# Performance work log

Hardware: AMD Instinct MI355X
Metric: run time of the kernel (lower is better)

## Reference

```python
import jax, jax.numpy as jnp
import numpy as np

LMAX = 4
S2_DIM = (LMAX + 1) ** 2                                  # 25: s2 irreps, mul 1 per l
SO3_DIM = sum((2 * l + 1) ** 2 for l in range(LMAX + 1))  # 165: so3 irreps, mul 2l+1 per l
B = 2048
F_S2, F_SO3 = 1, 16
N_S2_KERNEL = 48      # s2_healpix_grid(rec_level=1)
N_SO3_KERNEL = 192    # so3_near_identity_grid()
N_ACT_GRID = 4000     # SO3Activation resolution=10, aspect_ratio=2 -> 20x10x20, flattened
N_EVAL = 4608         # so3_healpix_grid(rec_level=2): 192 pixels x 24 gamma


def setup_inputs() -> dict:
    ks = jax.random.split(jax.random.key(0), 7)
    return {
        "x": jax.random.normal(ks[0], (B, F_S2, S2_DIM), jnp.float32),
        "w_s2": jax.random.normal(ks[1], (F_S2, F_SO3, N_S2_KERNEL), jnp.float32),
        "Y": jax.random.normal(ks[2], (N_S2_KERNEL, S2_DIM), jnp.float32),
        "w_so3": jax.random.normal(ks[3], (F_SO3, 1, N_SO3_KERNEL), jnp.float32),
        "D_kernel": jax.random.normal(ks[4], (N_SO3_KERNEL, SO3_DIM), jnp.float32),
        "D_act": jax.random.normal(ks[5], (N_ACT_GRID, SO3_DIM), jnp.float32),
        "eval_wigners": jax.random.normal(ks[6], (SO3_DIM, N_EVAL), jnp.float32) / np.sqrt(SO3_DIM),
    }


def _s2_to_so3_linear(x, psi):
    # e3nn o3.Linear(s2_irreps -> so3_irreps, f_in, f_out, external weights)
    # x:   [B, f_in, 25]  (mul 1 per degree l)
    # psi: [f_in, f_out, 25] ; column l^2+j is the weight to output-multiplicity j of degree l
    f_in, f_out = psi.shape[0], psi.shape[1]
    out, s = [], 0
    for l in range(LMAX + 1):
        d = 2 * l + 1
        x_l = x[..., s:s + d]                       # [B, f_in, d]
        p_l = psi[..., s:s + d]                     # [f_in, f_out, d] (j = out-mul idx)
        o = jnp.einsum('bxm,xyj->byjm', x_l, p_l) / np.sqrt(f_in)
        out.append(o.reshape(x.shape[0], f_out, d * d))
        s += d
    return jnp.concatenate(out, axis=-1)            # [B, f_out, 165]


def _so3_to_so3_linear(x, psi):
    # e3nn o3.Linear(so3_irreps -> so3_irreps, f_in, f_out, external weights)
    # x:   [B, f_in, 165] ; psi: [f_in, f_out, 165]
    f_in, f_out = psi.shape[0], psi.shape[1]
    out, s = [], 0
    for l in range(LMAX + 1):
        d = 2 * l + 1
        x_l = x[..., s:s + d * d].reshape(x.shape[0], f_in, d, d)   # [B,f_in,u,m]
        p_l = psi[..., s:s + d * d].reshape(f_in, f_out, d, d)      # [f_in,f_out,u,v]
        o = jnp.einsum('bxum,xyuv->byvm', x_l, p_l) / np.sqrt(f_in * d)
        out.append(o.reshape(x.shape[0], f_out, d * d))
        s += d * d
    return jnp.concatenate(out, axis=-1)            # [B, f_out, 165]


def _forward(x, w_s2, Y, w_so3, D_kernel, D_act, eval_wigners):
    # --- S2Convolution: kernel = SH-transform of grid weights, then irrep-wise linear
    psi1 = jnp.einsum('ni,xyn->xyi', Y, w_s2) / np.sqrt(N_S2_KERNEL)     # [1,16,25]
    h = _s2_to_so3_linear(x, psi1)                                        # [B,16,165]
    # --- SO3Activation: Fourier -> SO(3) grid -> relu -> Fourier
    g = jnp.einsum('bfi,gi->bfg', h, D_act) / np.sqrt(SO3_DIM)            # [B,16,4000]
    g = jax.nn.relu(g)
    h = jnp.einsum('bfg,gi->bfi', g, D_act) * (np.sqrt(SO3_DIM) / N_ACT_GRID)
    # --- SO3Convolution
    psi2 = jnp.einsum('ni,xyn->xyi', D_kernel, w_so3) / np.sqrt(N_SO3_KERNEL)  # [16,1,165]
    harmonics = _so3_to_so3_linear(h, psi2)                               # [B,1,165]
    # --- compute_probabilities: matmul with eval Wigner-D basis + softmax over grid
    probs = jax.nn.softmax(jnp.einsum('bfi,ie->be', harmonics, eval_wigners), axis=1)  # [B,4608]
    # --- top-k masking: zero out everything below the 5th-highest prob of sample 0
    fifth = jax.lax.top_k(probs, 5)[0][0, 4]
    probs = jnp.where(probs < fifth, 0.0, probs)
    return harmonics, probs


def reference(x, w_s2, Y, w_so3, D_kernel, D_act, eval_wigners):
    return _forward(x, w_s2, Y, w_so3, D_kernel, D_act, eval_wigners)
```

## Files before the change

kernel.cpp:

```cpp
#include <hip/hip_runtime.h>

typedef short bf16x8 __attribute__((ext_vector_type(8)));
typedef float f32x16 __attribute__((ext_vector_type(16)));
typedef int   i32x4  __attribute__((ext_vector_type(4)));

#define INV_SQRT165 0.07784989441615349f
#define FINAL_SCALE 0.0032113081446662823f
#define ZERO16 ((f32x16){0.f,0.f,0.f,0.f,0.f,0.f,0.f,0.f,0.f,0.f,0.f,0.f,0.f,0.f,0.f,0.f})

__device__ __forceinline__ unsigned short f2bf(float f) {
  unsigned int u = __builtin_bit_cast(unsigned int, f);
  unsigned int r = (u + 0x7FFFu + ((u >> 16) & 1u)) >> 16;
  return (unsigned short)r;
}
__device__ __forceinline__ float bf2f(unsigned short h) {
  unsigned int u = ((unsigned int)h) << 16;
  return __builtin_bit_cast(float, u);
}
__device__ __forceinline__ unsigned int pack_bf2f(float lo, float hi) {
  unsigned int a = (__builtin_bit_cast(unsigned int, lo) + 0x8000u) >> 16;
  unsigned int b = (__builtin_bit_cast(unsigned int, hi) + 0x8000u) & 0xFFFF0000u;
  return b | a;
}

__device__ __forceinline__ void gl_lds16(const void* g, void* l) {
  __builtin_amdgcn_global_load_lds(
      (const __attribute__((address_space(1))) unsigned int*)(unsigned long long)g,
      (__attribute__((address_space(3))) unsigned int*)(unsigned int)(unsigned long long)l,
      16, 0, 0);
}

__device__ __forceinline__ void decode_i(int i, int& lv, int& rel) {
  if (i < 1)       { lv = 0; rel = i; }
  else if (i < 10) { lv = 1; rel = i - 1; }
  else if (i < 35) { lv = 2; rel = i - 10; }
  else if (i < 84) { lv = 3; rel = i - 35; }
  else             { lv = 4; rel = i - 84; }
}
__device__ __forceinline__ int divq(int rel, int lv) {
  const int mag[5] = {32768, 10923, 6554, 4682, 3641};
  return (rel * mag[lv]) >> 15;
}

__device__ __forceinline__ int gperm(int p) {
  int a = p & 3, hlp = (p >> 2) & 1, c = p >> 3;
  return ((c >> 1) << 4) + hlp * 8 + ((c & 1) << 2) + a;
}

__global__ __launch_bounds__(256) void prep_k(const float* __restrict__ Da,
                                              const float* __restrict__ ew,
                                              const float* __restrict__ Y,
                                              const float* __restrict__ w_s2,
                                              const float* __restrict__ Dk,
                                              const float* __restrict__ w_so3,
                                              unsigned short* __restrict__ e1pre,
                                              unsigned short* __restrict__ d2pre,
                                              unsigned short* __restrict__ ewpre,
                                              float* __restrict__ psi2) {
  __shared__ __align__(16) unsigned short lds[13824];
  const int tid = threadIdx.x;
  const int l = tid & 63, hl = l >> 5, ln = l & 31;
  if (blockIdx.x < 128) {
    const int ci = blockIdx.x, g0 = ci * 32;
    float* psi1L = (float*)(lds + 6464);
    for (int e = tid; e < 6400; e += 256) lds[e] = 0;
    for (int e = tid; e < 400; e += 256) {
      int yv = e / 25, iv = e % 25;
      float s = 0.f;
      for (int n = 0; n < 48; n++) s += Y[n * 25 + iv] * w_s2[yv * 48 + n];
      psi1L[e] = s * 0.14433756729740643f;
    }
    __syncthreads();
    int rows = 4000 - g0; if (rows > 32) rows = 32; if (rows < 0) rows = 0;
    int ne = rows * 165;
    for (int e = tid; e < ne; e += 256) {
      int gl_ = e / 165, k = e - gl_ * 165;
      lds[gl_ * 200 + k] = f2bf(Da[g0 * 165 + e]);
    }
    __syncthreads();
#pragma unroll
    for (int it = 0; it < 3; it++) {
      int tt = it * 4 + (tid >> 6);
      int nf = tt >> 1, gk = tt & 1;
      unsigned short v[8];
#pragma unroll
      for (int j = 0; j < 8; j++)
        v[j] = lds[(gk * 16 + hl * 8 + j) * 200 + nf * 32 + ln];
      *(i32x4*)(d2pre + ci * 6144 + tt * 512 + l * 8) = *(i32x4*)v;
    }
    for (int yy = 0; yy < 16; yy++) {
#pragma unroll
      for (int it = 0; it < 4; it++) {
        int idx = it * 256 + tid;
        int kf = idx >> 9, r2 = idx & 511;
        int ll = r2 >> 3, j = r2 & 7;
        int lnn = ll & 31, hll = ll >> 5;
        int k = kf * 16 + hll * 8 + j;
        unsigned short ov = 0;
        if (k < 25) {
          int lv = (k < 1) ? 0 : (k < 4) ? 1 : (k < 9) ? 2 : (k < 16) ? 3 : 4;
          int d = 2 * lv + 1;
          int m = k - lv * lv;
          int off165 = lv * (4 * lv * lv - 1) / 3;
          int gp = gperm(lnn);
          float s = 0.f;
          const float* pr = psi1L + yy * 25 + lv * lv;
          const unsigned short* dr = lds + gp * 200 + off165 + m;
          for (int j2 = 0; j2 < d; j2++) s += pr[j2] * bf2f(dr[j2 * d]);
          ov = f2bf(s * INV_SQRT165);
        }
        e1pre[((yy * 128 + ci) * 2 + kf) * 512 + ll * 8 + j] = ov;
      }
    }
  } else if (blockIdx.x < 200) {
    const int bx2 = blockIdx.x - 128;
    const int n0 = bx2 * 64;
    for (int e = tid; e < 13824; e += 256) lds[e] = 0;
    __syncthreads();
    for (int e = tid; e < 10560; e += 256) {
      int k = e >> 6, n = e & 63;
      lds[k * 72 + n] = f2bf(ew[k * 4608 + n0 + n]);
    }
    __syncthreads();
#pragma unroll
    for (int it = 0; it < 6; it++) {
      int tb = it * 4 + (tid >> 6);
      int nt2 = tb / 12, kf = tb - nt2 * 12;
      unsigned short v[8];
#pragma unroll
      for (int j = 0; j < 8; j++)
        v[j] = lds[(kf * 16 + hl * 8 + j) * 72 + nt2 * 32 + ln];
      *(i32x4*)(ewpre + (bx2 * 2 + nt2) * 6144 + kf * 512 + l * 8) = *(i32x4*)v;
    }
  } else {
    int t = (blockIdx.x - 200) * 256 + tid;
    if (t < 2640) {
      int ch = t / 165, i = t % 165;
      float s = 0.f;
      for (int n = 0; n < 192; n++) s += Dk[n * 165 + i] * w_so3[ch * 192 + n];
      psi2[t] = s * (0.07216878364870323f * FINAL_SCALE);
    }
  }
}

__global__ __launch_bounds__(256, 3) void fused_mlp_k(
    const float* __restrict__ x,
    const unsigned short* __restrict__ e1pre,
    const unsigned short* __restrict__ d2pre,
    unsigned short* __restrict__ part)
{
  __shared__ __align__(16) unsigned char smem[28672];
  const int tid = threadIdx.x;
  const int w = tid >> 6, l = tid & 63;
  const int hl = l >> 5, ln = l & 31;
  const int h = blockIdx.x >> 8;
  const int y = (blockIdx.x >> 4) & 15;
  const int btg = blockIdx.x & 15;
  const int bt = btg * 4 + w;
  const int c0 = (h == 0) ? 0 : (h == 1) ? 43 : 86;
  const int cnt = (h == 2) ? 42 : 43;

  bf16x8 xf[2];
  {
    const float* xr = x + (bt * 32 + ln) * 25;
#pragma unroll
    for (int kf = 0; kf < 2; kf++) {
      unsigned short v[8];
#pragma unroll
      for (int j = 0; j < 8; j++) {
        int k = kf * 16 + hl * 8 + j;
        v[j] = (k < 25) ? f2bf(xr[k]) : (unsigned short)0;
      }
      xf[kf] = *(bf16x8*)v;
    }
  }

  f32x16 o[6];
#pragma unroll
  for (int i = 0; i < 6; i++) o[i] = ZERO16;

  const unsigned short* ebase = e1pre + (y * 128) * 1024;

#pragma unroll
  for (int i = 0; i < 4; i++) {
    int tb = w * 4 + i;
    if (tb < 14) {
      const unsigned short* g = (tb < 12) ? (d2pre + c0 * 6144 + tb * 512 + l * 8)
                                          : (ebase + (c0 * 2 + (tb - 12)) * 512 + l * 8);
      gl_lds16(g, smem + tb * 1024);
    }
  }

  for (int ci = 0; ci < cnt; ci++) {
    __syncthreads();
    const unsigned char* cb = smem + (ci & 1) * 14336;
    if (ci + 1 < cnt) {
      unsigned char* nb = smem + ((ci + 1) & 1) * 14336;
      const int c = c0 + ci + 1;
#pragma unroll
      for (int i = 0; i < 4; i++) {
        int tb = w * 4 + i;
        if (tb < 14) {
          const unsigned short* g = (tb < 12) ? (d2pre + c * 6144 + tb * 512 + l * 8)
                                              : (ebase + (c * 2 + (tb - 12)) * 512 + l * 8);
          gl_lds16(g, nb + tb * 1024);
        }
      }
    }
    bf16x8 aE0 = *(const bf16x8*)(cb + 12288 + l * 16);
    bf16x8 aE1 = *(const bf16x8*)(cb + 13312 + l * 16);
    f32x16 s = ZERO16;
    s = __builtin_amdgcn_mfma_f32_32x32x16_bf16(aE0, xf[0], s, 0, 0, 0);
    s = __builtin_amdgcn_mfma_f32_32x32x16_bf16(aE1, xf[1], s, 0, 0, 0);
    unsigned int dw[8];
#pragma unroll
    for (int p = 0; p < 8; p++)
      dw[p] = pack_bf2f(fmaxf(s[2 * p], 0.f), fmaxf(s[2 * p + 1], 0.f));
    i32x4 q0 = (i32x4){(int)dw[0], (int)dw[1], (int)dw[2], (int)dw[3]};
    i32x4 q1 = (i32x4){(int)dw[4], (int)dw[5], (int)dw[6], (int)dw[7]};
    bf16x8 a20 = __builtin_bit_cast(bf16x8, q0);
    bf16x8 a21 = __builtin_bit_cast(bf16x8, q1);
#pragma unroll
    for (int gk = 0; gk < 2; gk++) {
      bf16x8 a2 = gk ? a21 : a20;
#pragma unroll
      for (int nf = 0; nf < 6; nf++) {
        bf16x8 b2 = *(const bf16x8*)(cb + (nf * 2 + gk) * 1024 + l * 16);
        o[nf] = __builtin_amdgcn_mfma_f32_32x32x16_bf16(a2, b2, o[nf], 0, 0, 0);
      }
    }
  }

  unsigned short* pp = part + (size_t)((h * 16 + y) * 2048 + bt * 32) * 192;
#pragma unroll
  for (int nf = 0; nf < 6; nf++) {
    int n = nf * 32 + ln;
    if (n < 176) {
#pragma unroll
      for (int r = 0; r < 16; r++) {
        int row = (r & 3) + 8 * (r >> 2) + 4 * hl;
        pp[row * 192 + n] = f2bf(o[nf][r]);
      }
    }
  }
}

__global__ __launch_bounds__(256) void so3_k(const unsigned short* __restrict__ part,
                                             const float* __restrict__ psi2,
                                             float* __restrict__ harm_out,
                                             unsigned short* __restrict__ harmbpre) {
  __shared__ float lds[4 * 16 * 180];
  __shared__ float p2s[2640];
  const int tid = threadIdx.x;
  const int b0 = blockIdx.x * 4;
  for (int e = tid; e < 2640; e += 256) p2s[e] = psi2[e];
  {
    const int ybl = tid >> 2;
    const int yy = ybl & 15, bloc = ybl >> 4;
    const int s = tid & 3;
    const unsigned int* r0 = (const unsigned int*)(part + ((size_t)(0 * 16 + yy) * 2048 + b0 + bloc) * 192);
    const unsigned int* r1 = (const unsigned int*)(part + ((size_t)(1 * 16 + yy) * 2048 + b0 + bloc) * 192);
    const unsigned int* r2 = (const unsigned int*)(part + ((size_t)(2 * 16 + yy) * 2048 + b0 + bloc) * 192);
    float* dst = lds + (bloc * 16 + yy) * 180;
#pragma unroll
    for (int t = 0; t < 22; t++) {
      int d = s * 22 + t;
      if (d < 88) {
        unsigned int u0 = r0[d], u1 = r1[d], u2 = r2[d];
        int n0 = d * 2;
        dst[n0]     = bf2f((unsigned short)(u0 & 0xFFFF)) + bf2f((unsigned short)(u1 & 0xFFFF))
                    + bf2f((unsigned short)(u2 & 0xFFFF));
        dst[n0 + 1] = bf2f((unsigned short)(u0 >> 16)) + bf2f((unsigned short)(u1 >> 16))
                    + bf2f((unsigned short)(u2 >> 16));
      }
    }
  }
  __syncthreads();
  for (int jj = tid; jj < 768; jj += 256) {
    int e = (jj * 683) >> 17;
    int i = jj - e * 192;
    int bb = b0 + e;
    unsigned short* hb = harmbpre + (((bb >> 5) * 12 + (i >> 4)) << 9)
                       + ((i >> 3) & 1) * 256 + (bb & 31) * 8 + (i & 7);
    if (i < 165) {
      const float* row0 = lds + e * (16 * 180);
      int lv, rel; decode_i(i, lv, rel);
      int d = 2 * lv + 1;
      int off = i - rel;
      int v = divq(rel, lv), m = rel - v * d;
      float s = 0.f;
      for (int ch = 0; ch < 16; ch++) {
        const float* rw = row0 + ch * 180 + off;
        const float* p2 = p2s + ch * 165 + off;
        for (int u = 0; u < d; u++) s += rw[u * d + m] * p2[u * d + v];
      }
      s *= 0.25f * rsqrtf((float)d);
      harm_out[bb * 165 + i] = s;
      *hb = f2bf(s);
    } else {
      *hb = 0;
    }
  }
}

__global__ __launch_bounds__(64) void eval_k(
    const unsigned short* __restrict__ harmbpre,
    const unsigned short* __restrict__ ewpre,
    float* __restrict__ logits,
    float* __restrict__ logit0)
{
  const int l = threadIdx.x;
  const int hl = l >> 5, ln = l & 31;
  const int mt = blockIdx.y;
  const int n0 = blockIdx.x * 192;

  bf16x8 a[12];
  const short* ap = (const short*)harmbpre + mt * 6144 + l * 8;
#pragma unroll
  for (int kf = 0; kf < 12; kf++) a[kf] = *(const bf16x8*)(ap + kf * 512);

  f32x16 acc[6];
#pragma unroll
  for (int nf = 0; nf < 6; nf++) acc[nf] = ZERO16;

  const short* bp = (const short*)ewpre + (blockIdx.x * 6) * 6144 + l * 8;
#pragma unroll
  for (int kf = 0; kf < 12; kf++) {
#pragma unroll
    for (int nf = 0; nf < 6; nf++) {
      bf16x8 b = *(const bf16x8*)(bp + nf * 6144 + kf * 512);
      acc[nf] = __builtin_amdgcn_mfma_f32_32x32x16_bf16(a[kf], b, acc[nf], 0, 0, 0);
    }
  }
#pragma unroll
  for (int nf = 0; nf < 6; nf++) {
    const int col = n0 + nf * 32 + ln;
#pragma unroll
    for (int r = 0; r < 16; r++) {
      int row = (r & 3) + 8 * (r >> 2) + 4 * hl;
      logits[(mt * 32 + row) * 4608 + col] = acc[nf][r];
    }
  }
  if (mt == 0 && hl == 0) {
#pragma unroll
    for (int nf = 0; nf < 6; nf++) logit0[n0 + nf * 32 + ln] = acc[nf][0];
  }
}

__global__ __launch_bounds__(256) void smthresh_k(float* __restrict__ probs,
                                                  const float* __restrict__ logit0) {
  __shared__ float buf[4608];
  __shared__ float sm[8], ss[8];
  __shared__ float wv[4]; __shared__ int wi[4];
  __shared__ float gbest;
  float* p = probs + (size_t)blockIdx.x * 4608;
  const int tid = threadIdx.x;
  const int l = tid & 63, w = tid >> 6;
  float v[18];
  float mx = -3.4e38f, mx0 = -3.4e38f;
#pragma unroll
  for (int i = 0; i < 18; i++) {
    v[i] = p[i * 256 + tid];
    float t0 = logit0[i * 256 + tid];
    buf[i * 256 + tid] = t0;
    mx = fmaxf(mx, v[i]);
    mx0 = fmaxf(mx0, t0);
  }
#pragma unroll
  for (int off = 32; off >= 1; off >>= 1) {
    mx = fmaxf(mx, __shfl_xor(mx, off));
    mx0 = fmaxf(mx0, __shfl_xor(mx0, off));
  }
  if (l == 0) { sm[w] = mx; sm[4 + w] = mx0; }
  __syncthreads();
  mx  = fmaxf(fmaxf(sm[0], sm[1]), fmaxf(sm[2], sm[3]));
  mx0 = fmaxf(fmaxf(sm[4], sm[5]), fmaxf(sm[6], sm[7]));
  float s = 0.f, s0 = 0.f;
#pragma unroll
  for (int i = 0; i < 18; i++) {
    v[i] = __expf(v[i] - mx); s += v[i];
    s0 += __expf(buf[i * 256 + tid] - mx0);
  }
#pragma unroll
  for (int off = 32; off >= 1; off >>= 1) { s += __shfl_xor(s, off); s0 += __shfl_xor(s0, off); }
  if (l == 0) { ss[w] = s; ss[4 + w] = s0; }
  __syncthreads();
  s  = ss[0] + ss[1] + ss[2] + ss[3];
  s0 = ss[4] + ss[5] + ss[6] + ss[7];
  float inv = 1.f / s, inv0 = 1.f / s0;

  float ff = 0.f;
  for (int it = 0; it < 5; it++) {
    float bm = -3.4e38f; int bi = 0;
    for (int i = tid; i < 4608; i += 256) {
      float xx = buf[i];
      if (xx > bm) { bm = xx; bi = i; }
    }
    for (int off = 32; off >= 1; off >>= 1) {
      float ov = __shfl_xor(bm, off); int oi = __shfl_xor(bi, off);
      if (ov > bm) { bm = ov; bi = oi; }
    }
    if (l == 0) { wv[w] = bm; wi[w] = bi; }
    __syncthreads();
    if (tid == 0) {
      float B = wv[0]; int I = wi[0];
      for (int k = 1; k < 4; k++) if (wv[k] > B) { B = wv[k]; I = wi[k]; }
      gbest = B;
      buf[I] = -3.4e38f;
    }
    __syncthreads();
    ff = gbest;
    __syncthreads();
  }
  float t = __expf(ff - mx0) * inv0;
#pragma unroll
  for (int i = 0; i < 18; i++) {
    float pv = v[i] * inv;
    p[i * 256 + tid] = (pv < t) ? 0.f : pv;
  }
}

extern "C" void kernel_launch(void* const* d_in, const int* in_sizes, int n_in,
                              void* d_out, int out_size, void* d_ws, size_t ws_size,
                              hipStream_t stream) {
  const float* x     = (const float*)d_in[0];
  const float* w_s2  = (const float*)d_in[1];
  const float* Y     = (const float*)d_in[2];
  const float* w_so3 = (const float*)d_in[3];
  const float* Dk    = (const float*)d_in[4];
  const float* Da    = (const float*)d_in[5];
  const float* ew    = (const float*)d_in[6];

  float* out = (float*)d_out;
  float* harm_out = out;
  float* probs    = out + 337920;
  unsigned short* part = (unsigned short*)probs;

  char* ws = (char*)d_ws;
  float* psi2  = (float*)(ws + 0);
  unsigned short* e1pre    = (unsigned short*)(ws + 12288);
  unsigned short* d2pre    = (unsigned short*)(ws + 4206592);
  unsigned short* ewpre    = (unsigned short*)(ws + 5779456);
  unsigned short* harmbpre = (unsigned short*)(ws + 7548928);
  float* logit0 = (float*)(ws + 8335360);

  prep_k<<<211, 256, 0, stream>>>(Da, ew, Y, w_s2, Dk, w_so3, e1pre, d2pre, ewpre, psi2);
  fused_mlp_k<<<768, 256, 0, stream>>>(x, e1pre, d2pre, part);
  so3_k<<<512, 256, 0, stream>>>(part, psi2, harm_out, harmbpre);
  eval_k<<<dim3(24, 64), 64, 0, stream>>>(harmbpre, ewpre, probs, logit0);
  smthresh_k<<<2048, 256, 0, stream>>>(probs, logit0);
}
```

Measured before the change: 235.3 us.

## Split prep e1 work across more blocks, load E tiles to registers, compact partial stride

The prep kernel now splits each chunk's 16 output-channel loop across four blocks, giving 512 instead of 128 blocks so the weight pre-transform runs with more parallelism, at the cost of redundantly reloading Da and psi1 per block. In the fused MLP kernel the E1 fragments are read straight from global memory into registers with one-step prefetch instead of being staged through LDS, which shrinks shared memory and removes the uneven per-warp load guard. The partial-sum buffer row stride drops from 192 to 176 elements, cutting write and read traffic between the MLP and SO3 kernels.

Result: faster. 220.3 us (-6.4%).

```diff
diff --git a/kernel.cpp b/kernel.cpp
--- a/kernel.cpp
+++ b/kernel.cpp
@@ -60,8 +60,9 @@
   __shared__ __align__(16) unsigned short lds[13824];
   const int tid = threadIdx.x;
   const int l = tid & 63, hl = l >> 5, ln = l & 31;
-  if (blockIdx.x < 128) {
-    const int ci = blockIdx.x, g0 = ci * 32;
+  if (blockIdx.x < 512) {
+    const int ci = blockIdx.x >> 2, yg = blockIdx.x & 3;
+    const int g0 = ci * 32;
     float* psi1L = (float*)(lds + 6464);
     for (int e = tid; e < 6400; e += 256) lds[e] = 0;
     for (int e = tid; e < 400; e += 256) {
@@ -78,17 +79,20 @@
       lds[gl_ * 200 + k] = f2bf(Da[g0 * 165 + e]);
     }
     __syncthreads();
-#pragma unroll
-    for (int it = 0; it < 3; it++) {
-      int tt = it * 4 + (tid >> 6);
-      int nf = tt >> 1, gk = tt & 1;
-      unsigned short v[8];
-#pragma unroll
-      for (int j = 0; j < 8; j++)
-        v[j] = lds[(gk * 16 + hl * 8 + j) * 200 + nf * 32 + ln];
-      *(i32x4*)(d2pre + ci * 6144 + tt * 512 + l * 8) = *(i32x4*)v;
-    }
-    for (int yy = 0; yy < 16; yy++) {
+    if (yg == 0) {
+#pragma unroll
+      for (int it = 0; it < 3; it++) {
+        int tt = it * 4 + (tid >> 6);
+        int nf = tt >> 1, gk = tt & 1;
+        unsigned short v[8];
+#pragma unroll
+        for (int j = 0; j < 8; j++)
+          v[j] = lds[(gk * 16 + hl * 8 + j) * 200 + nf * 32 + ln];
+        *(i32x4*)(d2pre + ci * 6144 + tt * 512 + l * 8) = *(i32x4*)v;
+      }
+    }
+    for (int yi = 0; yi < 4; yi++) {
+      int yy = yg * 4 + yi;
 #pragma unroll
       for (int it = 0; it < 4; it++) {
         int idx = it * 256 + tid;
@@ -112,8 +116,8 @@
         e1pre[((yy * 128 + ci) * 2 + kf) * 512 + ll * 8 + j] = ov;
       }
     }
-  } else if (blockIdx.x < 200) {
-    const int bx2 = blockIdx.x - 128;
+  } else if (blockIdx.x < 584) {
+    const int bx2 = blockIdx.x - 512;
     const int n0 = bx2 * 64;
     for (int e = tid; e < 13824; e += 256) lds[e] = 0;
     __syncthreads();
@@ -133,7 +137,7 @@
       *(i32x4*)(ewpre + (bx2 * 2 + nt2) * 6144 + kf * 512 + l * 8) = *(i32x4*)v;
     }
   } else {
-    int t = (blockIdx.x - 200) * 256 + tid;
+    int t = (blockIdx.x - 584) * 256 + tid;
     if (t < 2640) {
       int ch = t / 165, i = t % 165;
       float s = 0.f;
@@ -149,7 +153,7 @@
     const unsigned short* __restrict__ d2pre,
     unsigned short* __restrict__ part)
 {
-  __shared__ __align__(16) unsigned char smem[28672];
+  __shared__ __align__(16) unsigned char smem[24576];
   const int tid = threadIdx.x;
   const int w = tid >> 6, l = tid & 63;
   const int hl = l >> 5, ln = l & 31;
@@ -181,37 +185,32 @@
 
   const unsigned short* ebase = e1pre + (y * 128) * 1024;
 
-#pragma unroll
-  for (int i = 0; i < 4; i++) {
-    int tb = w * 4 + i;
-    if (tb < 14) {
-      const unsigned short* g = (tb < 12) ? (d2pre + c0 * 6144 + tb * 512 + l * 8)
-                                          : (ebase + (c0 * 2 + (tb - 12)) * 512 + l * 8);
-      gl_lds16(g, smem + tb * 1024);
-    }
+  bf16x8 eC0 = *(const bf16x8*)(ebase + (c0 * 2 + 0) * 512 + l * 8);
+  bf16x8 eC1 = *(const bf16x8*)(ebase + (c0 * 2 + 1) * 512 + l * 8);
+#pragma unroll
+  for (int i = 0; i < 3; i++) {
+    int tb = w * 3 + i;
+    gl_lds16(d2pre + c0 * 6144 + tb * 512 + l * 8, smem + tb * 1024);
   }
 
   for (int ci = 0; ci < cnt; ci++) {
     __syncthreads();
-    const unsigned char* cb = smem + (ci & 1) * 14336;
+    const unsigned char* cb = smem + (ci & 1) * 12288;
+    bf16x8 eN0 = eC0, eN1 = eC1;
     if (ci + 1 < cnt) {
-      unsigned char* nb = smem + ((ci + 1) & 1) * 14336;
+      unsigned char* nb = smem + ((ci + 1) & 1) * 12288;
       const int c = c0 + ci + 1;
 #pragma unroll
-      for (int i = 0; i < 4; i++) {
-        int tb = w * 4 + i;
-        if (tb < 14) {
-          const unsigned short* g = (tb < 12) ? (d2pre + c * 6144 + tb * 512 + l * 8)
-                                              : (ebase + (c * 2 + (tb - 12)) * 512 + l * 8);
-          gl_lds16(g, nb + tb * 1024);
-        }
-      }
-    }
-    bf16x8 aE0 = *(const bf16x8*)(cb + 12288 + l * 16);
-    bf16x8 aE1 = *(const bf16x8*)(cb + 13312 + l * 16);
+      for (int i = 0; i < 3; i++) {
+        int tb = w * 3 + i;
+        gl_lds16(d2pre + c * 6144 + tb * 512 + l * 8, nb + tb * 1024);
+      }
+      eN0 = *(const bf16x8*)(ebase + (c * 2 + 0) * 512 + l * 8);
+      eN1 = *(const bf16x8*)(ebase + (c * 2 + 1) * 512 + l * 8);
+    }
     f32x16 s = ZERO16;
-    s = __builtin_amdgcn_mfma_f32_32x32x16_bf16(aE0, xf[0], s, 0, 0, 0);
-    s = __builtin_amdgcn_mfma_f32_32x32x16_bf16(aE1, xf[1], s, 0, 0, 0);
+    s = __builtin_amdgcn_mfma_f32_32x32x16_bf16(eC0, xf[0], s, 0, 0, 0);
+    s = __builtin_amdgcn_mfma_f32_32x32x16_bf16(eC1, xf[1], s, 0, 0, 0);
     unsigned int dw[8];
 #pragma unroll
     for (int p = 0; p < 8; p++)
@@ -229,9 +228,10 @@
         o[nf] = __builtin_amdgcn_mfma_f32_32x32x16_bf16(a2, b2, o[nf], 0, 0, 0);
       }
     }
-  }
-
-  unsigned short* pp = part + (size_t)((h * 16 + y) * 2048 + bt * 32) * 192;
+    eC0 = eN0; eC1 = eN1;
+  }
+
+  unsigned short* pp = part + (size_t)((h * 16 + y) * 2048 + bt * 32) * 176;
 #pragma unroll
   for (int nf = 0; nf < 6; nf++) {
     int n = nf * 32 + ln;
@@ -239,7 +239,7 @@
 #pragma unroll
       for (int r = 0; r < 16; r++) {
         int row = (r & 3) + 8 * (r >> 2) + 4 * hl;
-        pp[row * 192 + n] = f2bf(o[nf][r]);
+        pp[row * 176 + n] = f2bf(o[nf][r]);
       }
     }
   }
@@ -258,21 +258,19 @@
     const int ybl = tid >> 2;
     const int yy = ybl & 15, bloc = ybl >> 4;
     const int s = tid & 3;
-    const unsigned int* r0 = (const unsigned int*)(part + ((size_t)(0 * 16 + yy) * 2048 + b0 + bloc) * 192);
-    const unsigned int* r1 = (const unsigned int*)(part + ((size_t)(1 * 16 + yy) * 2048 + b0 + bloc) * 192);
-    const unsigned int* r2 = (const unsigned int*)(part + ((size_t)(2 * 16 + yy) * 2048 + b0 + bloc) * 192);
+    const unsigned int* r0 = (const unsigned int*)(part + ((size_t)(0 * 16 + yy) * 2048 + b0 + bloc) * 176);
+    const unsigned int* r1 = (const unsigned int*)(part + ((size_t)(1 * 16 + yy) * 2048 + b0 + bloc) * 176);
+    const unsigned int* r2 = (const unsigned int*)(part + ((size_t)(2 * 16 + yy) * 2048 + b0 + bloc) * 176);
     float* dst = lds + (bloc * 16 + yy) * 180;
 #pragma unroll
     for (int t = 0; t < 22; t++) {
       int d = s * 22 + t;
-      if (d < 88) {
-        unsigned int u0 = r0[d], u1 = r1[d], u2 = r2[d];
-        int n0 = d * 2;
-        dst[n0]     = bf2f((unsigned short)(u0 & 0xFFFF)) + bf2f((unsigned short)(u1 & 0xFFFF))
-                    + bf2f((unsigned short)(u2 & 0xFFFF));
-        dst[n0 + 1] = bf2f((unsigned short)(u0 >> 16)) + bf2f((unsigned short)(u1 >> 16))
-                    + bf2f((unsigned short)(u2 >> 16));
-      }
+      unsigned int u0 = r0[d], u1 = r1[d], u2 = r2[d];
+      int n0 = d * 2;
+      dst[n0]     = bf2f((unsigned short)(u0 & 0xFFFF)) + bf2f((unsigned short)(u1 & 0xFFFF))
+                  + bf2f((unsigned short)(u2 & 0xFFFF));
+      dst[n0 + 1] = bf2f((unsigned short)(u0 >> 16)) + bf2f((unsigned short)(u1 >> 16))
+                  + bf2f((unsigned short)(u2 >> 16));
     }
   }
   __syncthreads();
@@ -444,7 +442,7 @@
   unsigned short* harmbpre = (unsigned short*)(ws + 7548928);
   float* logit0 = (float*)(ws + 8335360);
 
-  prep_k<<<211, 256, 0, stream>>>(Da, ew, Y, w_s2, Dk, w_so3, e1pre, d2pre, ewpre, psi2);
+  prep_k<<<595, 256, 0, stream>>>(Da, ew, Y, w_s2, Dk, w_so3, e1pre, d2pre, ewpre, psi2);
   fused_mlp_k<<<768, 256, 0, stream>>>(x, e1pre, d2pre, part);
   so3_k<<<512, 256, 0, stream>>>(part, psi2, harm_out, harmbpre);
   eval_k<<<dim3(24, 64), 64, 0, stream>>>(harmbpre, ewpre, probs, logit0);
```
